# Kernel tuning notes

Measured on AMD Instinct MI355X. Metric: run time of the kernel, lower is better.

## Reference

```python
import jax, jax.numpy as jnp
import numpy as np

N, F_IN, H, C = 8192, 1024, 512, 64

def setup_inputs() -> dict:
    key = jax.random.key(0)
    k1, k2, k3, k4, k5, k6 = jax.random.split(key, 6)
    X = jax.random.normal(k1, (N, F_IN), dtype=jnp.float32)
    tilde = jax.random.uniform(k2, (N, N), dtype=jnp.float32)
    # torch.nn.Linear params, stored as [in, out] for direct matmul
    W1 = jax.random.normal(k3, (F_IN, H), dtype=jnp.float32) * (1.0 / np.sqrt(F_IN))
    b1 = jax.random.normal(k4, (H,), dtype=jnp.float32) * 0.01
    W2 = jax.random.normal(k5, (H, C), dtype=jnp.float32) * (1.0 / np.sqrt(H))
    b2 = jax.random.normal(k6, (C,), dtype=jnp.float32) * 0.01
    return {"X": X, "tilde": tilde, "W1": W1, "b1": b1, "W2": W2, "b2": b2}

def reference(X, tilde, W1, b1, W2, b2):
    # normalize(): D1 = col sums, D2 = row sums; torch broadcasting applies
    # BOTH [N] vectors over the column axis: A[i,j] = sqrt(D1[j])*tilde[i,j]*sqrt(D2[j])
    D1 = jnp.sum(tilde, axis=0)  # [N]
    D2 = jnp.sum(tilde, axis=1)  # [N]
    scale = jnp.sqrt(D1) * jnp.sqrt(D2)  # [N], column scaling
    A = tilde * scale[None, :]  # [N, N] normalized adjacency
    # Layer 1: Linear then propagate, ReLU
    h = jax.nn.relu(A @ (X @ W1 + b1))  # [N, H]
    # Layer 2: Linear then propagate
    out = A @ (h @ W2 + b2)  # [N, C]
    return out
```

## Files before the change

kernel.cpp:

```cpp
#include <hip/hip_runtime.h>
#include <hip/hip_bf16.h>
#include <cstdint>
#include <cstddef>

typedef __attribute__((ext_vector_type(8))) __bf16 bf16x8;
typedef __attribute__((ext_vector_type(4))) float f32x4;
typedef __attribute__((ext_vector_type(4))) unsigned short u16x4;

#define DEVINL static __device__ __forceinline__

DEVINL unsigned short f2bf(float x) {
  union { float f; unsigned u; } un; un.f = x;
  unsigned r = un.u + 0x7fffu + ((un.u >> 16) & 1u);
  return (unsigned short)(r >> 16);
}

DEVINL float bf2f(unsigned short b) {
  union { unsigned u; float f; } un; un.u = ((unsigned)b) << 16;
  return un.f;
}

DEVINL void gload16(const void* g, void* l) {
  __builtin_amdgcn_global_load_lds(
      (__attribute__((address_space(1))) void*)(void*)(uintptr_t)(const void*)g,
      (__attribute__((address_space(3))) void*)l, 16, 0, 0);
}

#define SBAR() asm volatile("s_barrier" ::: "memory")
#define WLG0() asm volatile("s_waitcnt lgkmcnt(0)" ::: "memory")
#define WVM6() asm volatile("s_waitcnt vmcnt(6)" ::: "memory")

__global__ __launch_bounds__(256, 2) void sums_convert(const float* __restrict__ tilde,
                                                       float4* __restrict__ partials4,
                                                       float* __restrict__ D2,
                                                       u16x4* __restrict__ Tbf) {
  const int t = threadIdx.x;
  float4 ca[8];
#pragma unroll
  for (int i = 0; i < 8; ++i) ca[i] = (float4){0.f, 0.f, 0.f, 0.f};
  float rs[16];
#pragma unroll
  for (int r = 0; r < 16; ++r) rs[r] = 0.f;

  const int base_row = blockIdx.x * 16;
  for (int r = 0; r < 16; ++r) {
    const size_t rowoff = (size_t)(base_row + r) * 2048;
    const float4* rp = (const float4*)tilde + rowoff;
    u16x4* op = Tbf + rowoff;
#pragma unroll
    for (int i = 0; i < 8; ++i) {
      float4 v = rp[t + i * 256];
      ca[i].x += v.x; ca[i].y += v.y; ca[i].z += v.z; ca[i].w += v.w;
      rs[r] += (v.x + v.y) + (v.z + v.w);
      u16x4 o;
      o[0] = f2bf(v.x); o[1] = f2bf(v.y); o[2] = f2bf(v.z); o[3] = f2bf(v.w);
      op[t + i * 256] = o;
    }
  }
  float4* pb = partials4 + (size_t)blockIdx.x * 2048;
#pragma unroll
  for (int i = 0; i < 8; ++i) pb[t + i * 256] = ca[i];

#pragma unroll
  for (int r = 0; r < 16; ++r) {
#pragma unroll
    for (int off = 32; off > 0; off >>= 1) rs[r] += __shfl_down(rs[r], off, 64);
  }
  __shared__ float wsum[4][16];
  const int wave = t >> 6;
  if ((t & 63) == 0) {
#pragma unroll
    for (int r = 0; r < 16; ++r) wsum[wave][r] = rs[r];
  }
  __syncthreads();
  if (t < 16) D2[base_row + t] = wsum[0][t] + wsum[1][t] + wsum[2][t] + wsum[3][t];
}

__global__ __launch_bounds__(256) void zreduce(const float4* __restrict__ partials4,
                                               float4* __restrict__ partials2_4) {
  const int c4 = blockIdx.x * 256 + threadIdx.x;
  const int z0 = blockIdx.y * 8;
  float4 s = (float4){0.f, 0.f, 0.f, 0.f};
#pragma unroll
  for (int z = z0; z < z0 + 8; ++z) {
    float4 v = partials4[(size_t)z * 2048 + c4];
    s.x += v.x; s.y += v.y; s.z += v.z; s.w += v.w;
  }
  partials2_4[(size_t)blockIdx.y * 2048 + c4] = s;
}

__global__ __launch_bounds__(256) void colscale_kernel(const float* __restrict__ partials2,
                                                       const float* __restrict__ D2,
                                                       float* __restrict__ sv) {
  int j = blockIdx.x * 256 + threadIdx.x;
  float d1 = 0.f;
  for (int z = 0; z < 64; ++z) d1 += partials2[z * 8192 + j];
  sv[j] = sqrtf(d1 * D2[j]);
}

__global__ __launch_bounds__(256) void prep_fused(const float4* __restrict__ X4,
                                                  u16x4* __restrict__ Xbf4,
                                                  const float* __restrict__ W1,
                                                  unsigned short* __restrict__ W1T,
                                                  const float* __restrict__ W2,
                                                  unsigned short* __restrict__ W2T) {
  const int b = blockIdx.x;
  if (b < 2048) {
    const int n4 = 8192 * 1024 / 4;
    for (int i = b * 256 + threadIdx.x; i < n4; i += 2048 * 256) {
      float4 v = X4[i];
      u16x4 o;
      o[0] = f2bf(v.x); o[1] = f2bf(v.y); o[2] = f2bf(v.z); o[3] = f2bf(v.w);
      Xbf4[i] = o;
    }
  } else if (b < 4096) {
    int o = (b - 2048) * 256 + threadIdx.x;
    int c = o >> 10, r = o & 1023;
    W1T[o] = f2bf(W1[(size_t)r * 512 + c]);
  } else {
    int o = (b - 4096) * 256 + threadIdx.x;
    int c = o >> 9, r = o & 511;
    W2T[o] = f2bf(W2[(size_t)r * 64 + c]);
  }
}

__global__ __launch_bounds__(512, 2) void gemm2_8ph(
    const unsigned short* __restrict__ A,
    const unsigned short* __restrict__ BT,
    unsigned short* __restrict__ Cpart) {
  constexpr int K = 8192;
  constexpr int LDC = 512;
  constexpr int NT = 32;

  __shared__ __align__(16) char lds[131072];

  const int tid = threadIdx.x;
  const int lane = tid & 63, w = tid >> 6;
  const int wr = w >> 2, wc = w & 3;
  const int lrow = lane & 15, slot = lane >> 4;
  const int xorv = (((lrow >> 2) & 1) << 5) | (((lrow >> 3) & 1) << 6);
  const int row0 = blockIdx.x * 256;
  const int col0 = blockIdx.y * 256;
  const size_t kbeg = (size_t)blockIdx.z * 2048;

  f32x4 acc[8][4];
#pragma unroll
  for (int m = 0; m < 8; ++m)
#pragma unroll
    for (int n = 0; n < 4; ++n) acc[m][n] = (f32x4){0.f, 0.f, 0.f, 0.f};
  bf16x8 a[4][2], b[4][2];

  auto STAGE_A = [&](int buf, int h, int tk) {
    if (tk >= NT) return;
    const size_t kabs = kbeg + (size_t)tk * 64;
    char* dst = lds + buf * 65536;
#pragma unroll
    for (int j = 0; j < 2; ++j) {
      int L = h * 16384 + (j * 512 + tid) * 16;
      int y = L ^ ((L & 0x600) >> 4);
      int lam = y >> 7, cb = y & 127;
      int R = ((lam >> 6) & 1) * 128 + (lam >> 7) * 64 + (lam & 63);
      gload16((const char*)A + ((size_t)(row0 + R) * K + kabs) * 2 + cb, dst + L);
    }
  };
  auto STAGE_B = [&](int buf, int h, int tk) {
    if (tk >= NT) return;
    const size_t kabs = kbeg + (size_t)tk * 64;
    char* dst = lds + buf * 65536 + 32768;
#pragma unroll
    for (int j = 0; j < 2; ++j) {
      int L = h * 16384 + (j * 512 + tid) * 16;
      int y = L ^ ((L & 0x600) >> 4);
      int lam = y >> 7, cb = y & 127;
      int R = ((lam >> 5) & 3) * 64 + (lam >> 7) * 32 + (lam & 31);
      gload16((const char*)BT + ((size_t)(col0 + R) * K + kabs) * 2 + cb, dst + L);
    }
  };
  auto LDA = [&](int buf, int mh) {
    const char* base = lds + buf * 65536;
#pragma unroll
    for (int mm = 0; mm < 4; ++mm)
#pragma unroll
      for (int ks = 0; ks < 2; ++ks) {
        int lin = mh * 16384 + wr * 8192 + mm * 2048 + lrow * 128 + ks * 64 + slot * 16;
        a[mm][ks] = *(const bf16x8*)(base + (lin ^ xorv));
      }
  };
  auto LDB = [&](int buf, int nh) {
    const char* base = lds + buf * 65536 + 32768;
#pragma unroll
    for (int nn = 0; nn < 2; ++nn)
#pragma unroll
      for (int ks = 0; ks < 2; ++ks) {
        int lin = nh * 16384 + wc * 4096 + nn * 2048 + lrow * 128 + ks * 64 + slot * 16;
        b[nh * 2 + nn][ks] = *(const bf16x8*)(base + (lin ^ xorv));
      }
  };
  auto MMA = [&](int mh, int nh) {
    __builtin_amdgcn_s_setprio(1);
#pragma unroll
    for (int mm = 0; mm < 4; ++mm)
#pragma unroll
      for (int nn = 0; nn < 2; ++nn)
#pragma unroll
        for (int ks = 0; ks < 2; ++ks)
          acc[mh * 4 + mm][nh * 2 + nn] = __builtin_amdgcn_mfma_f32_16x16x32_bf16(
              a[mm][ks], b[nh * 2 + nn][ks], acc[mh * 4 + mm][nh * 2 + nn], 0, 0, 0);
    __builtin_amdgcn_s_setprio(0);
  };

  STAGE_A(0, 0, 0); STAGE_B(0, 0, 0); STAGE_B(0, 1, 0); STAGE_A(0, 1, 0);
  STAGE_A(1, 0, 1); STAGE_B(1, 0, 1); STAGE_B(1, 1, 1);
  WVM6(); SBAR();

  for (int it = 0; it < NT / 2; ++it) {
    const int t = 2 * it;
    LDA(0, 0); LDB(0, 0);
    STAGE_A(1, 1, t + 1);
    SBAR(); WLG0();
    MMA(0, 0);
    SBAR();
    LDB(0, 1);
    STAGE_A(0, 0, t + 2);
    SBAR(); WLG0();
    MMA(0, 1);
    SBAR();
    LDA(0, 1);
    STAGE_B(0, 0, t + 2);
    SBAR(); WLG0();
    MMA(1, 1);
    SBAR();
    STAGE_B(0, 1, t + 2);
    WVM6();
    SBAR();
    MMA(1, 0);
    SBAR();
    LDA(1, 0); LDB(1, 0);
    STAGE_A(0, 1, t + 2);
    SBAR(); WLG0();
    MMA(0, 0);
    SBAR();
    LDB(1, 1);
    STAGE_A(1, 0, t + 3);
    SBAR(); WLG0();
    MMA(0, 1);
    SBAR();
    LDA(1, 1);
    STAGE_B(1, 0, t + 3);
    SBAR(); WLG0();
    MMA(1, 1);
    SBAR();
    STAGE_B(1, 1, t + 3);
    WVM6();
    SBAR();
    MMA(1, 0);
    SBAR();
  }

  unsigned short* Cb = Cpart + (size_t)blockIdx.z * 8192 * LDC;
  const int r0 = row0 + wr * 128, c0 = col0 + wc * 64;
#pragma unroll
  for (int m = 0; m < 8; ++m)
#pragma unroll
    for (int n = 0; n < 4; ++n)
#pragma unroll
      for (int j = 0; j < 4; ++j) {
        int row = r0 + m * 16 + (lane >> 4) * 4 + j;
        int col = c0 + n * 16 + lrow;
        Cb[(size_t)row * LDC + col] = f2bf(acc[m][n][j]);
      }
}

template <int BM, int BN, int EPI>
__global__ __launch_bounds__(256) void gemm_bt(
    const unsigned short* __restrict__ A,
    const unsigned short* __restrict__ BT,
    void* __restrict__ C,
    const float* __restrict__ bias,
    const float* __restrict__ cs,
    int M, int N, int K, int kChunk, int ldc) {
  constexpr int WTM = BM / 2, WTN = BN / 2;
  constexpr int MR = WTM / 16, NR = WTN / 16;
  constexpr int AIT = BM * 4 / 256;
  constexpr int BIT = BN * 4 / 256;

  __shared__ unsigned short As[BM * 32];
  __shared__ unsigned short Bs[BN * 32];

  const int t = threadIdx.x;
  const int lane = t & 63, wave = t >> 6;
  const int wr = wave >> 1, wc = wave & 1;
  const int bm = blockIdx.x, bn = blockIdx.y, bz = blockIdx.z;
  const int row0 = bm * BM, col0 = bn * BN;
  const int kbeg = bz * kChunk, kend = kbeg + kChunk;
  const int lrow = lane & 15;
  const int lk = (lane >> 4) * 8;

  f32x4 acc[MR][NR];
#pragma unroll
  for (int m = 0; m < MR; ++m)
#pragma unroll
    for (int n = 0; n < NR; ++n) acc[m][n] = (f32x4){0.f, 0.f, 0.f, 0.f};

  for (int k0 = kbeg; k0 < kend; k0 += 32) {
#pragma unroll
    for (int i = 0; i < AIT; ++i) {
      int flat = i * 256 + t;
      int r = flat >> 2, ko = (flat & 3) * 8;
      gload16(A + (size_t)(row0 + r) * K + k0 + ko, As + (size_t)flat * 8);
    }
#pragma unroll
    for (int i = 0; i < BIT; ++i) {
      int flat = i * 256 + t;
      int r = flat >> 2, ko = (flat & 3) * 8;
      gload16(BT + (size_t)(col0 + r) * K + k0 + ko, Bs + (size_t)flat * 8);
    }
    __syncthreads();

    bf16x8 af[MR], bfr[NR];
#pragma unroll
    for (int m = 0; m < MR; ++m)
      af[m] = *(const bf16x8*)&As[(wr * WTM + m * 16 + lrow) * 32 + lk];
#pragma unroll
    for (int n = 0; n < NR; ++n)
      bfr[n] = *(const bf16x8*)&Bs[(wc * WTN + n * 16 + lrow) * 32 + lk];
#pragma unroll
    for (int m = 0; m < MR; ++m)
#pragma unroll
      for (int n = 0; n < NR; ++n)
        acc[m][n] = __builtin_amdgcn_mfma_f32_16x16x32_bf16(af[m], bfr[n], acc[m][n], 0, 0, 0);
    __syncthreads();
  }

  const int r0 = row0 + wr * WTM, c0 = col0 + wc * WTN;
  if constexpr (EPI == 2) {
    float* Cf = (float*)C + (size_t)bz * M * ldc;
#pragma unroll
    for (int m = 0; m < MR; ++m)
#pragma unroll
      for (int n = 0; n < NR; ++n)
#pragma unroll
        for (int j = 0; j < 4; ++j) {
          int row = r0 + m * 16 + (lane >> 4) * 4 + j;
          int col = c0 + n * 16 + lrow;
          Cf[(size_t)row * ldc + col] = acc[m][n][j];
        }
  } else if constexpr (EPI == 4) {
    unsigned short* Cb = (unsigned short*)C + (size_t)bz * M * ldc;
#pragma unroll
    for (int m = 0; m < MR; ++m)
#pragma unroll
      for (int n = 0; n < NR; ++n)
#pragma unroll
        for (int j = 0; j < 4; ++j) {
          int row = r0 + m * 16 + (lane >> 4) * 4 + j;
          int col = c0 + n * 16 + lrow;
          Cb[(size_t)row * ldc + col] = f2bf(acc[m][n][j]);
        }
  } else {
    unsigned short* Cb = (unsigned short*)C;
#pragma unroll
    for (int m = 0; m < MR; ++m)
#pragma unroll
      for (int n = 0; n < NR; ++n)
#pragma unroll
        for (int j = 0; j < 4; ++j) {
          int row = r0 + m * 16 + (lane >> 4) * 4 + j;
          int col = c0 + n * 16 + lrow;
          float v = acc[m][n][j];
          if constexpr (EPI == 1) v = v > 0.f ? v : 0.f;
          if constexpr (EPI == 3) v = (v + bias[row]) * cs[col];
          Cb[(size_t)row * ldc + col] = f2bf(v);
        }
  }
}

__global__ __launch_bounds__(256) void reduce_relu_b16p(const u16x4* __restrict__ part,
                                                        u16x4* __restrict__ out,
                                                        int total4, int splits) {
  const int stride = gridDim.x * 256;
  for (int i = blockIdx.x * 256 + threadIdx.x; i < total4; i += stride) {
    float s0 = 0.f, s1 = 0.f, s2 = 0.f, s3 = 0.f;
    for (int z = 0; z < splits; ++z) {
      u16x4 v = part[(size_t)z * total4 + i];
      s0 += bf2f(v[0]); s1 += bf2f(v[1]); s2 += bf2f(v[2]); s3 += bf2f(v[3]);
    }
    u16x4 o;
    o[0] = f2bf(s0 > 0.f ? s0 : 0.f);
    o[1] = f2bf(s1 > 0.f ? s1 : 0.f);
    o[2] = f2bf(s2 > 0.f ? s2 : 0.f);
    o[3] = f2bf(s3 > 0.f ? s3 : 0.f);
    out[i] = o;
  }
}

__global__ __launch_bounds__(256) void reduce_zt(const float4* __restrict__ part,
                                                 const float* __restrict__ b2,
                                                 const float* __restrict__ sv,
                                                 u16x4* __restrict__ out) {
  const int i4 = blockIdx.x * 256 + threadIdx.x;
  const int row = i4 >> 11;
  const int col0 = (i4 & 2047) * 4;
  float4 s = part[i4];
#pragma unroll
  for (int z = 1; z < 4; ++z) {
    float4 v = part[(size_t)z * 131072 + i4];
    s.x += v.x; s.y += v.y; s.z += v.z; s.w += v.w;
  }
  const float b = b2[row];
  u16x4 o;
  o[0] = f2bf((s.x + b) * sv[col0 + 0]);
  o[1] = f2bf((s.y + b) * sv[col0 + 1]);
  o[2] = f2bf((s.z + b) * sv[col0 + 2]);
  o[3] = f2bf((s.w + b) * sv[col0 + 3]);
  out[i4] = o;
}

__global__ __launch_bounds__(256) void reduce_out(const u16x4* __restrict__ part,
                                                  float4* __restrict__ out,
                                                  int total4, int splits) {
  const int i = blockIdx.x * 256 + threadIdx.x;
  if (i >= total4) return;
  float s0 = 0.f, s1 = 0.f, s2 = 0.f, s3 = 0.f;
  for (int z = 0; z < splits; ++z) {
    u16x4 v = part[(size_t)z * total4 + i];
    s0 += bf2f(v[0]); s1 += bf2f(v[1]); s2 += bf2f(v[2]); s3 += bf2f(v[3]);
  }
  out[i] = (float4){s0, s1, s2, s3};
}

extern "C" void kernel_launch(void* const* d_in, const int* in_sizes, int n_in,
                              void* d_out, int out_size, void* d_ws, size_t ws_size,
                              hipStream_t stream) {
  const float* X     = (const float*)d_in[0];
  const float* tilde = (const float*)d_in[1];
  const float* W1    = (const float*)d_in[2];
  const float* b1    = (const float*)d_in[3];
  const float* W2    = (const float*)d_in[4];
  const float* b2    = (const float*)d_in[5];
  float* out = (float*)d_out;

  constexpr int N = 8192, F = 1024, H = 512, Cc = 64;

  char* ws = (char*)d_ws;
  size_t off = 0;
  auto alloc = [&](size_t bytes) {
    char* p = ws + off;
    off += (bytes + 255) & ~(size_t)255;
    return p;
  };
  unsigned short* Tbf  = (unsigned short*)alloc((size_t)N * N * 2);
  unsigned short* XW1T = (unsigned short*)alloc((size_t)H * N * 2);
  unsigned short* hbuf = (unsigned short*)alloc((size_t)N * H * 2);
  unsigned short* ZT   = (unsigned short*)alloc((size_t)Cc * N * 2);
  unsigned short* W2T  = (unsigned short*)alloc((size_t)Cc * H * 2);
  float* partials2 = (float*)alloc(64 * N * 4);
  float* D2 = (float*)alloc(N * 4);
  float* sv = (float*)alloc(N * 4);
  const size_t scratch_base = off;
  unsigned short* Xbf = (unsigned short*)(ws + scratch_base);
  unsigned short* W1T = (unsigned short*)(ws + scratch_base + (size_t)N * F * 2);
  float* partials = (float*)(ws + scratch_base + (size_t)N * F * 2 + 0x200000);
  unsigned short* part2 = (unsigned short*)(ws + scratch_base);
  float* part3 = (float*)(ws + scratch_base);
  unsigned short* part4 = (unsigned short*)(ws + scratch_base);

  const size_t need_split =
      scratch_base + (size_t)N * F * 2 + 0x200000 + (size_t)512 * N * 4;
  const bool splitk = ws_size >= need_split;

  sums_convert<<<512, 256, 0, stream>>>(tilde, (float4*)partials, D2, (u16x4*)Tbf);
  zreduce<<<dim3(8, 64), 256, 0, stream>>>((const float4*)partials, (float4*)partials2);
  colscale_kernel<<<N / 256, 256, 0, stream>>>(partials2, D2, sv);

  prep_fused<<<4224, 256, 0, stream>>>((const float4*)X, (u16x4*)Xbf, W1, W1T, W2, W2T);

  gemm_bt<64, 128, 3><<<dim3(H / 64, N / 128, 1), 256, 0, stream>>>(
      W1T, Xbf, XW1T, b1, sv, H, N, F, F, N);

  if (splitk) {
    gemm2_8ph<<<dim3(N / 256, H / 256, 4), 512, 0, stream>>>(Tbf, XW1T, part2);
    reduce_relu_b16p<<<1024, 256, 0, stream>>>((const u16x4*)part2, (u16x4*)hbuf,
                                               N * H / 4, 4);
    gemm_bt<64, 128, 2><<<dim3(1, N / 128, 4), 256, 0, stream>>>(
        W2T, hbuf, part3, nullptr, nullptr, Cc, N, H, H / 4, N);
    reduce_zt<<<(Cc * N / 4) / 256, 256, 0, stream>>>((const float4*)part3, b2, sv,
                                                      (u16x4*)ZT);
    gemm_bt<128, 64, 4><<<dim3(N / 128, 1, 8), 256, 0, stream>>>(
        Tbf, ZT, part4, nullptr, nullptr, N, Cc, N, N / 8, Cc);
    reduce_out<<<(N * Cc / 4) / 256, 256, 0, stream>>>((const u16x4*)part4, (float4*)out,
                                                       N * Cc / 4, 8);
  } else {
    gemm_bt<128, 128, 1><<<dim3(N / 128, H / 128, 1), 256, 0, stream>>>(
        Tbf, XW1T, hbuf, nullptr, nullptr, N, H, N, N, H);
    gemm_bt<64, 128, 3><<<dim3(1, N / 128, 1), 256, 0, stream>>>(
        W2T, hbuf, ZT, b2, sv, Cc, N, H, H, N);
    gemm_bt<128, 64, 4><<<dim3(N / 128, 1, 1), 256, 0, stream>>>(
        Tbf, ZT, part4, nullptr, nullptr, N, Cc, N, N, Cc);
    reduce_out<<<(N * Cc / 4) / 256, 256, 0, stream>>>((const u16x4*)part4, (float4*)out,
                                                       N * Cc / 4, 1);
  }
}
```

Before: 259.9 us.

## Fuse split-K reduce+ReLU into layer-2 GEMM, merge zreduce into prep, remap gemm2 blocks per XCD

Folds the column-sum z-reduction into the prep kernel, removing one launch. The split-K reduction and ReLU of the big propagation GEMM now happen while loading the B tile of the small W2 GEMM, so the separate reduce_relu kernel and its hbuf round-trip are gone. gemm2 also switches to a 1D grid with an XCD-aware block remap, so neighbouring row tiles land on the same XCD and can share L2. The costs are that the fused GEMM rereads all four bf16 partials per block, part3 moves to a separate scratch region, and the fallback path changes to a plain GEMM followed by reduce_zt.

```diff
diff --git a/kernel.cpp b/kernel.cpp
--- a/kernel.cpp
+++ b/kernel.cpp
@@ -6,6 +6,7 @@
 typedef __attribute__((ext_vector_type(8))) __bf16 bf16x8;
 typedef __attribute__((ext_vector_type(4))) float f32x4;
 typedef __attribute__((ext_vector_type(4))) unsigned short u16x4;
+typedef __attribute__((ext_vector_type(8))) unsigned short u16x8;
 
 #define DEVINL static __device__ __forceinline__
 
@@ -76,17 +77,43 @@
   if (t < 16) D2[base_row + t] = wsum[0][t] + wsum[1][t] + wsum[2][t] + wsum[3][t];
 }
 
-__global__ __launch_bounds__(256) void zreduce(const float4* __restrict__ partials4,
-                                               float4* __restrict__ partials2_4) {
-  const int c4 = blockIdx.x * 256 + threadIdx.x;
-  const int z0 = blockIdx.y * 8;
-  float4 s = (float4){0.f, 0.f, 0.f, 0.f};
-#pragma unroll
-  for (int z = z0; z < z0 + 8; ++z) {
-    float4 v = partials4[(size_t)z * 2048 + c4];
-    s.x += v.x; s.y += v.y; s.z += v.z; s.w += v.w;
-  }
-  partials2_4[(size_t)blockIdx.y * 2048 + c4] = s;
+__global__ __launch_bounds__(256) void prep_fused(const float4* __restrict__ partials4,
+                                                  float4* __restrict__ partials2_4,
+                                                  const float4* __restrict__ X4,
+                                                  u16x4* __restrict__ Xbf4,
+                                                  const float* __restrict__ W1,
+                                                  unsigned short* __restrict__ W1T,
+                                                  const float* __restrict__ W2,
+                                                  unsigned short* __restrict__ W2T) {
+  const int b = blockIdx.x;
+  if (b < 512) {
+    const int bx = b & 7, by = b >> 3;
+    const int c4 = bx * 256 + threadIdx.x;
+    const int z0 = by * 8;
+    float4 s = (float4){0.f, 0.f, 0.f, 0.f};
+#pragma unroll
+    for (int z = z0; z < z0 + 8; ++z) {
+      float4 v = partials4[(size_t)z * 2048 + c4];
+      s.x += v.x; s.y += v.y; s.z += v.z; s.w += v.w;
+    }
+    partials2_4[(size_t)by * 2048 + c4] = s;
+  } else if (b < 2560) {
+    const int n4 = 8192 * 1024 / 4;
+    for (int i = (b - 512) * 256 + threadIdx.x; i < n4; i += 2048 * 256) {
+      float4 v = X4[i];
+      u16x4 o;
+      o[0] = f2bf(v.x); o[1] = f2bf(v.y); o[2] = f2bf(v.z); o[3] = f2bf(v.w);
+      Xbf4[i] = o;
+    }
+  } else if (b < 4608) {
+    int o = (b - 2560) * 256 + threadIdx.x;
+    int c = o >> 10, r = o & 1023;
+    W1T[o] = f2bf(W1[(size_t)r * 512 + c]);
+  } else {
+    int o = (b - 4608) * 256 + threadIdx.x;
+    int c = o >> 9, r = o & 511;
+    W2T[o] = f2bf(W2[(size_t)r * 64 + c]);
+  }
 }
 
 __global__ __launch_bounds__(256) void colscale_kernel(const float* __restrict__ partials2,
@@ -98,32 +125,6 @@
   sv[j] = sqrtf(d1 * D2[j]);
 }
 
-__global__ __launch_bounds__(256) void prep_fused(const float4* __restrict__ X4,
-                                                  u16x4* __restrict__ Xbf4,
-                                                  const float* __restrict__ W1,
-                                                  unsigned short* __restrict__ W1T,
-                                                  const float* __restrict__ W2,
-                                                  unsigned short* __restrict__ W2T) {
-  const int b = blockIdx.x;
-  if (b < 2048) {
-    const int n4 = 8192 * 1024 / 4;
-    for (int i = b * 256 + threadIdx.x; i < n4; i += 2048 * 256) {
-      float4 v = X4[i];
-      u16x4 o;
-      o[0] = f2bf(v.x); o[1] = f2bf(v.y); o[2] = f2bf(v.z); o[3] = f2bf(v.w);
-      Xbf4[i] = o;
-    }
-  } else if (b < 4096) {
-    int o = (b - 2048) * 256 + threadIdx.x;
-    int c = o >> 10, r = o & 1023;
-    W1T[o] = f2bf(W1[(size_t)r * 512 + c]);
-  } else {
-    int o = (b - 4096) * 256 + threadIdx.x;
-    int c = o >> 9, r = o & 511;
-    W2T[o] = f2bf(W2[(size_t)r * 64 + c]);
-  }
-}
-
 __global__ __launch_bounds__(512, 2) void gemm2_8ph(
     const unsigned short* __restrict__ A,
     const unsigned short* __restrict__ BT,
@@ -139,9 +140,14 @@
   const int wr = w >> 2, wc = w & 3;
   const int lrow = lane & 15, slot = lane >> 4;
   const int xorv = (((lrow >> 2) & 1) << 5) | (((lrow >> 3) & 1) << 6);
-  const int row0 = blockIdx.x * 256;
-  const int col0 = blockIdx.y * 256;
-  const size_t kbeg = (size_t)blockIdx.z * 2048;
+  const int i = blockIdx.x;
+  const int xcd = i & 7, sl = i >> 3;
+  const int bx = xcd * 4 + (sl & 3);
+  const int yz = sl >> 2;
+  const int by = yz & 1, bz = yz >> 1;
+  const int row0 = bx * 256;
+  const int col0 = by * 256;
+  const size_t kbeg = (size_t)bz * 2048;
 
   f32x4 acc[8][4];
 #pragma unroll
@@ -257,7 +263,7 @@
     SBAR();
   }
 
-  unsigned short* Cb = Cpart + (size_t)blockIdx.z * 8192 * LDC;
+  unsigned short* Cb = Cpart + (size_t)bz * 8192 * LDC;
   const int r0 = row0 + wr * 128, c0 = col0 + wc * 64;
 #pragma unroll
   for (int m = 0; m < 8; ++m)
@@ -268,6 +274,84 @@
         int row = r0 + m * 16 + (lane >> 4) * 4 + j;
         int col = c0 + n * 16 + lrow;
         Cb[(size_t)row * LDC + col] = f2bf(acc[m][n][j]);
+      }
+}
+
+__global__ __launch_bounds__(256) void gemm3_fused(
+    const unsigned short* __restrict__ W2T,
+    const unsigned short* __restrict__ part2,
+    float* __restrict__ part3) {
+  constexpr int BM = 64, BN = 128, K = 512;
+  constexpr int PSTRIDE = 8192 * 512;
+  __shared__ unsigned short As[BM * 32];
+  __shared__ unsigned short Bs[BN * 32];
+
+  const int t = threadIdx.x;
+  const int lane = t & 63, wave = t >> 6;
+  const int wr = wave >> 1, wc = wave & 1;
+  const int col0 = blockIdx.y * BN;
+  const int kbeg = blockIdx.z * 128, kend = kbeg + 128;
+  const int lrow = lane & 15;
+  const int lk = (lane >> 4) * 8;
+
+  f32x4 acc[2][4];
+#pragma unroll
+  for (int m = 0; m < 2; ++m)
+#pragma unroll
+    for (int n = 0; n < 4; ++n) acc[m][n] = (f32x4){0.f, 0.f, 0.f, 0.f};
+
+  for (int k0 = kbeg; k0 < kend; k0 += 32) {
+    {
+      int r = t >> 2, ko = (t & 3) * 8;
+      gload16(W2T + (size_t)r * K + k0 + ko, As + (size_t)t * 8);
+    }
+#pragma unroll
+    for (int i = 0; i < 2; ++i) {
+      int flat = i * 256 + t;
+      int r = flat >> 2, ko = (flat & 3) * 8;
+      const size_t base = (size_t)(col0 + r) * K + k0 + ko;
+      float s[8];
+#pragma unroll
+      for (int e = 0; e < 8; ++e) s[e] = 0.f;
+#pragma unroll
+      for (int z = 0; z < 4; ++z) {
+        u16x8 v = *(const u16x8*)(part2 + (size_t)z * PSTRIDE + base);
+#pragma unroll
+        for (int e = 0; e < 8; ++e) s[e] += bf2f(v[e]);
+      }
+      u16x8 o;
+#pragma unroll
+      for (int e = 0; e < 8; ++e) o[e] = f2bf(s[e] > 0.f ? s[e] : 0.f);
+      *(u16x8*)&Bs[(size_t)flat * 8] = o;
+    }
+    __syncthreads();
+
+    bf16x8 af[2], bfr[4];
+#pragma unroll
+    for (int m = 0; m < 2; ++m)
+      af[m] = *(const bf16x8*)&As[(wr * 32 + m * 16 + lrow) * 32 + lk];
+#pragma unroll
+    for (int n = 0; n < 4; ++n)
+      bfr[n] = *(const bf16x8*)&Bs[(wc * 64 + n * 16 + lrow) * 32 + lk];
+#pragma unroll
+    for (int m = 0; m < 2; ++m)
+#pragma unroll
+      for (int n = 0; n < 4; ++n)
+        acc[m][n] = __builtin_amdgcn_mfma_f32_16x16x32_bf16(af[m], bfr[n], acc[m][n], 0, 0, 0);
+    __syncthreads();
+  }
+
+  float* Cf = part3 + (size_t)blockIdx.z * 64 * 8192;
+  const int r0 = wr * 32, c0 = col0 + wc * 64;
+#pragma unroll
+  for (int m = 0; m < 2; ++m)
+#pragma unroll
+    for (int n = 0; n < 4; ++n)
+#pragma unroll
+      for (int j = 0; j < 4; ++j) {
+        int row = r0 + m * 16 + (lane >> 4) * 4 + j;
+        int col = c0 + n * 16 + lrow;
+        Cf[(size_t)row * 8192 + col] = acc[m][n][j];
       }
 }
 
@@ -397,13 +481,13 @@
 __global__ __launch_bounds__(256) void reduce_zt(const float4* __restrict__ part,
                                                  const float* __restrict__ b2,
                                                  const float* __restrict__ sv,
-                                                 u16x4* __restrict__ out) {
+                                                 u16x4* __restrict__ out,
+                                                 int splits) {
   const int i4 = blockIdx.x * 256 + threadIdx.x;
   const int row = i4 >> 11;
   const int col0 = (i4 & 2047) * 4;
   float4 s = part[i4];
-#pragma unroll
-  for (int z = 1; z < 4; ++z) {
+  for (int z = 1; z < splits; ++z) {
     float4 v = part[(size_t)z * 131072 + i4];
     s.x += v.x; s.y += v.y; s.z += v.z; s.w += v.w;
   }
@@ -462,30 +546,25 @@
   unsigned short* W1T = (unsigned short*)(ws + scratch_base + (size_t)N * F * 2);
   float* partials = (float*)(ws + scratch_base + (size_t)N * F * 2 + 0x200000);
   unsigned short* part2 = (unsigned short*)(ws + scratch_base);
-  float* part3 = (float*)(ws + scratch_base);
+  float* part3 = (float*)(ws + scratch_base + (size_t)4 * N * H * 2);
   unsigned short* part4 = (unsigned short*)(ws + scratch_base);
 
-  const size_t need_split =
-      scratch_base + (size_t)N * F * 2 + 0x200000 + (size_t)512 * N * 4;
-  const bool splitk = ws_size >= need_split;
+  const size_t scratch_need = (size_t)4 * N * H * 2 + (size_t)4 * Cc * N * 4;
+  const bool splitk = ws_size >= scratch_base + scratch_need;
 
   sums_convert<<<512, 256, 0, stream>>>(tilde, (float4*)partials, D2, (u16x4*)Tbf);
-  zreduce<<<dim3(8, 64), 256, 0, stream>>>((const float4*)partials, (float4*)partials2);
+  prep_fused<<<4736, 256, 0, stream>>>((const float4*)partials, (float4*)partials2,
+                                       (const float4*)X, (u16x4*)Xbf, W1, W1T, W2, W2T);
   colscale_kernel<<<N / 256, 256, 0, stream>>>(partials2, D2, sv);
-
-  prep_fused<<<4224, 256, 0, stream>>>((const float4*)X, (u16x4*)Xbf, W1, W1T, W2, W2T);
 
   gemm_bt<64, 128, 3><<<dim3(H / 64, N / 128, 1), 256, 0, stream>>>(
       W1T, Xbf, XW1T, b1, sv, H, N, F, F, N);
 
   if (splitk) {
-    gemm2_8ph<<<dim3(N / 256, H / 256, 4), 512, 0, stream>>>(Tbf, XW1T, part2);
-    reduce_relu_b16p<<<1024, 256, 0, stream>>>((const u16x4*)part2, (u16x4*)hbuf,
-                                               N * H / 4, 4);
-    gemm_bt<64, 128, 2><<<dim3(1, N / 128, 4), 256, 0, stream>>>(
-        W2T, hbuf, part3, nullptr, nullptr, Cc, N, H, H / 4, N);
+    gemm2_8ph<<<256, 512, 0, stream>>>(Tbf, XW1T, part2);
+    gemm3_fused<<<dim3(1, N / 128, 4), 256, 0, stream>>>(W2T, part2, part3);
     reduce_zt<<<(Cc * N / 4) / 256, 256, 0, stream>>>((const float4*)part3, b2, sv,
-                                                      (u16x4*)ZT);
+                                                      (u16x4*)ZT, 4);
     gemm_bt<128, 64, 4><<<dim3(N / 128, 1, 8), 256, 0, stream>>>(
         Tbf, ZT, part4, nullptr, nullptr, N, Cc, N, N / 8, Cc);
     reduce_out<<<(N * Cc / 4) / 256, 256, 0, stream>>>((const u16x4*)part4, (float4*)out,
@@ -493,8 +572,10 @@
   } else {
     gemm_bt<128, 128, 1><<<dim3(N / 128, H / 128, 1), 256, 0, stream>>>(
         Tbf, XW1T, hbuf, nullptr, nullptr, N, H, N, N, H);
-    gemm_bt<64, 128, 3><<<dim3(1, N / 128, 1), 256, 0, stream>>>(
-        W2T, hbuf, ZT, b2, sv, Cc, N, H, H, N);
+    gemm_bt<64, 128, 2><<<dim3(1, N / 128, 1), 256, 0, stream>>>(
+        W2T, hbuf, part3, nullptr, nullptr, Cc, N, H, H, N);
+    reduce_zt<<<(Cc * N / 4) / 256, 256, 0, stream>>>((const float4*)part3, b2, sv,
+                                                      (u16x4*)ZT, 1);
     gemm_bt<128, 64, 4><<<dim3(N / 128, 1, 1), 256, 0, stream>>>(
         Tbf, ZT, part4, nullptr, nullptr, N, Cc, N, N, Cc);
     reduce_out<<<(N * Cc / 4) / 256, 256, 0, stream>>>((const u16x4*)part4, (float4*)out,
```

Result: no change. 255.0 us (-1.8%).
